# Optimization experiments

Measured on AMD Instinct MI355X. Metric: run time of the kernel, lower is better.

## Reference

```python
import jax, jax.numpy as jnp
import numpy as np

INPUT_DIM = 1024
HIDDEN = 64
NUM_MEM = 8   # +1 shared slot -> 9 total
K = 2
SEQ = 256
BATCH = 32


def setup_inputs() -> dict:
    key = jax.random.key(0)
    ks = jax.random.split(key, 10)
    s = 1.0 / np.sqrt(INPUT_DIM)
    nm1 = NUM_MEM + 1
    return {
        "X": jax.random.normal(ks[0], (SEQ, BATCH, INPUT_DIM), jnp.float32),
        "M_0": jnp.zeros((BATCH, nm1, HIDDEN, HIDDEN), jnp.float32),
        "Wk_w": jax.random.uniform(ks[1], (HIDDEN * nm1, INPUT_DIM), jnp.float32, -s, s),
        "Wk_b": jax.random.uniform(ks[2], (HIDDEN * nm1,), jnp.float32, -s, s),
        "Wv_w": jax.random.uniform(ks[3], (HIDDEN * nm1, INPUT_DIM), jnp.float32, -s, s),
        "Wv_b": jax.random.uniform(ks[4], (HIDDEN * nm1,), jnp.float32, -s, s),
        "Wg_w": jax.random.uniform(ks[5], (NUM_MEM, INPUT_DIM), jnp.float32, -s, s),
        "Wg_b": jax.random.uniform(ks[6], (NUM_MEM,), jnp.float32, -s, s),
        "Wq_w": jax.random.uniform(ks[7], (HIDDEN, INPUT_DIM), jnp.float32, -s, s),
        "Wq_b": jax.random.uniform(ks[8], (HIDDEN,), jnp.float32, -s, s),
    }


def _mom_forward(X, M_0, Wk_w, Wk_b, Wv_w, Wv_b, Wg_w, Wg_b, Wq_w, Wq_b):
    B = X.shape[1]
    nm1 = NUM_MEM + 1
    b_idx = jnp.arange(B)[:, None]

    def step(M, x_t):
        # gating + top-k routing (sorted descending, like torch.topk)
        score = jax.nn.softmax(x_t @ Wg_w.T + Wg_b, axis=1)          # (B, NUM_MEM)
        m_scores, m_idx = jax.lax.top_k(score, K)                    # (B, K)
        idx_update = jnp.concatenate(
            [jnp.zeros((B, 1), jnp.int32), m_idx.astype(jnp.int32)], axis=1)  # (B, K+1)
        g = m_scores / jnp.sum(m_scores, axis=1, keepdims=True)     # (B, K)

        Mk = (x_t @ Wk_w.T + Wk_b).reshape(B, nm1, HIDDEN)          # (B, 9, H)
        Mv = (x_t @ Wv_w.T + Wv_b).reshape(B, nm1, HIDDEN)
        # only gather the K+1 routed outer products instead of all 9
        k_sel = jnp.take_along_axis(Mk, idx_update[:, :, None], axis=1)  # (B, K+1, H)
        v_sel = jnp.take_along_axis(Mv, idx_update[:, :, None], axis=1)
        src = k_sel[..., :, None] * v_sel[..., None, :]              # (B, K+1, H, H)
        M = M.at[b_idx, idx_update].add(src)                         # scatter-add (dupes accumulate)

        M_use = M[b_idx, m_idx]                                      # (B, K, H, H)
        M_out = jnp.einsum('bk,bkij->bij', g, M_use) + M[:, 0]       # add shared memory
        q = x_t @ Wq_w.T + Wq_b                                      # (B, H)
        o = jnp.einsum('bi,bij->bj', q, M_out)                       # (B, H)
        return M, o

    M_final, outputs = jax.lax.scan(step, M_0, X)
    return outputs, M_final


def reference(X, M_0, Wk_w, Wk_b, Wv_w, Wv_b, Wg_w, Wg_b, Wq_w, Wq_b):
    return _mom_forward(X, M_0, Wk_w, Wk_b, Wv_w, Wv_b, Wg_w, Wg_b, Wq_w, Wq_b)
```

## Files before the change

kernel.cpp:

```cpp
#include <hip/hip_runtime.h>
#include <stdint.h>

#define SEQ 256
#define BATCH 32
#define IN_DIM 1024
#define HID 64
#define NPAD 1280
#define ROWS (SEQ*BATCH)

#define XBF_OFF   0
#define DMH_OFF   0
#define WBF_OFF   16777216
#define BB_OFF    19398656
#define GATE_OFF  19403776
#define Y_OFF     19534848

#define NC 8
#define CHL 32

#define DM_CB_U32 18432

typedef __attribute__((ext_vector_type(8))) short short8;
typedef __attribute__((ext_vector_type(4))) float floatx4;

typedef const __attribute__((address_space(1))) unsigned int gas_u32;
typedef __attribute__((address_space(3))) unsigned int las_u32;
static __device__ __forceinline__ void gl_lds16(const void* g, void* l) {
  __builtin_amdgcn_global_load_lds((gas_u32*)g, (las_u32*)l, 16, 0, 0);
}

static __device__ __forceinline__ short f2bf(float f) {
  union { float f; uint32_t u; } a; a.f = f;
  uint32_t r = (a.u + 0x7FFFu + ((a.u >> 16) & 1u)) >> 16;
  return (short)r;
}
static __device__ __forceinline__ float bflo(uint32_t u){ return __uint_as_float(u << 16); }
static __device__ __forceinline__ float bfhi(uint32_t u){ return __uint_as_float(u & 0xffff0000u); }
static __device__ __forceinline__ float bfu(unsigned short us){ return __uint_as_float(((uint32_t)us) << 16); }

__global__ __launch_bounds__(256) void prep_gate_kernel(
    const float* __restrict__ X,
    const float* __restrict__ Wk, const float* __restrict__ bk,
    const float* __restrict__ Wv, const float* __restrict__ bv,
    const float* __restrict__ Wg, const float* __restrict__ bg,
    const float* __restrict__ Wq, const float* __restrict__ bq,
    short* __restrict__ Xbf, short* __restrict__ Wbf,
    float* __restrict__ bb, float4* __restrict__ gate)
{
  if (blockIdx.x < 2048) {
    const int lane = threadIdx.x & 63;
    const int row  = blockIdx.x * 4 + (threadIdx.x >> 6);
    const float* x = X + (int64_t)row * IN_DIM;
    short4* xb = (short4*)(Xbf + (int64_t)row * IN_DIM);

    float acc[8];
#pragma unroll
    for (int e = 0; e < 8; e++) acc[e] = 0.f;
#pragma unroll
    for (int i = 0; i < 4; i++) {
      const int off = i * 256 + lane * 4;
      float4 xv = *(const float4*)(x + off);
      short4 s4;
      s4.x = f2bf(xv.x); s4.y = f2bf(xv.y); s4.z = f2bf(xv.z); s4.w = f2bf(xv.w);
      xb[i * 64 + lane] = s4;
#pragma unroll
      for (int e = 0; e < 8; e++) {
        float4 wv = *(const float4*)(Wg + e * IN_DIM + off);
        acc[e] += xv.x * wv.x + xv.y * wv.y + xv.z * wv.z + xv.w * wv.w;
      }
    }
#pragma unroll
    for (int e = 0; e < 8; e++) {
#pragma unroll
      for (int m = 32; m >= 1; m >>= 1)
        acc[e] += __shfl_xor(acc[e], m);
      acc[e] += bg[e];
    }
    if (lane == 0) {
      int i0 = 0; float v0 = acc[0];
#pragma unroll
      for (int e = 1; e < 8; e++) if (acc[e] > v0) { v0 = acc[e]; i0 = e; }
      int i1 = -1; float v1 = -3.4e38f;
#pragma unroll
      for (int e = 0; e < 8; e++) if (e != i0 && acc[e] > v1) { v1 = acc[e]; i1 = e; }
      float e1 = __expf(v1 - v0);
      float inv = 1.f / (1.f + e1);
      gate[row] = make_float4(__int_as_float(i0), __int_as_float(i1), inv, e1 * inv);
    }
  } else {
    const int idx = (blockIdx.x - 2048) * 256 + threadIdx.x;
    const int NW4 = NPAD * IN_DIM / 4;
#pragma unroll
    for (int i = idx; i < NW4; i += 65536) {
      int e = i * 4;
      int r = e >> 10;
      int k = e & 1023;
      float4 x;
      if (r < 576)       x = *(const float4*)(Wk + (int64_t)r*1024 + k);
      else if (r < 1152) x = *(const float4*)(Wv + (int64_t)(r-576)*1024 + k);
      else if (r < 1216) x = *(const float4*)(Wq + (int64_t)(r-1152)*1024 + k);
      else               x = make_float4(0.f, 0.f, 0.f, 0.f);
      short4 s4;
      s4.x = f2bf(x.x); s4.y = f2bf(x.y); s4.z = f2bf(x.z); s4.w = f2bf(x.w);
      ((short4*)Wbf)[i] = s4;
    }
    if (idx < NPAD) {
      int r = idx; float v;
      if (r < 576)       v = bk[r];
      else if (r < 1152) v = bv[r - 576];
      else if (r < 1216) v = bq[r - 1152];
      else               v = 0.f;
      bb[r] = v;
    }
  }
}

__global__ __launch_bounds__(256) void gemm_kernel(
    const short* __restrict__ Xbf,
    const short* __restrict__ Wbf,
    const float* __restrict__ bb,
    unsigned short* __restrict__ Yb)
{
  __shared__ short As[128 * 32];
  __shared__ short Bs[128 * 32];

  const int tid  = threadIdx.x;
  const int lane = tid & 63;
  const int wv   = tid >> 6;
  const int quad = lane >> 4;
  const int cl   = lane & 15;
  const int wm   = wv & 1;
  const int wn   = wv >> 1;
  const int m0 = blockIdx.y * 128;
  const int n0 = blockIdx.x * 128;

  const int srow = wv * 32 + (lane >> 2);
  const int scol = (lane & 3) * 8;
  const short* gA = Xbf + (int64_t)(m0 + srow) * IN_DIM + scol;
  const short* gB = Wbf + (int64_t)(n0 + srow) * IN_DIM + scol;
  short* lA = As + (wv * 32) * 32;
  short* lB = Bs + (wv * 32) * 32;

  floatx4 acc[4][4];
#pragma unroll
  for (int i = 0; i < 4; i++)
#pragma unroll
    for (int k = 0; k < 4; k++) acc[i][k] = (floatx4){0.f, 0.f, 0.f, 0.f};

  for (int ks = 0; ks < IN_DIM; ks += 32) {
    gl_lds16(gA + ks,                lA);
    gl_lds16(gA + 16 * IN_DIM + ks,  lA + 16 * 32);
    gl_lds16(gB + ks,                lB);
    gl_lds16(gB + 16 * IN_DIM + ks,  lB + 16 * 32);
    __syncthreads();

    short8 bfrag[4], afrag[4];
#pragma unroll
    for (int nt = 0; nt < 4; nt++)
      bfrag[nt] = *(const short8*)(&Bs[(wn * 64 + nt * 16 + cl) * 32 + quad * 8]);
#pragma unroll
    for (int mt = 0; mt < 4; mt++)
      afrag[mt] = *(const short8*)(&As[(wm * 64 + mt * 16 + cl) * 32 + quad * 8]);
#pragma unroll
    for (int mt = 0; mt < 4; mt++)
#pragma unroll
      for (int nt = 0; nt < 4; nt++)
        acc[mt][nt] = __builtin_amdgcn_mfma_f32_16x16x32_bf16(afrag[mt], bfrag[nt], acc[mt][nt], 0, 0, 0);
    __syncthreads();
  }

#pragma unroll
  for (int nt = 0; nt < 4; nt++) {
    const int col = n0 + wn * 64 + nt * 16 + cl;
    const float bias = bb[col];
#pragma unroll
    for (int mt = 0; mt < 4; mt++) {
#pragma unroll
      for (int r = 0; r < 4; r++) {
        int row = m0 + wm * 64 + mt * 16 + quad * 4 + r;
        Yb[(int64_t)row * NPAD + col] = (unsigned short)f2bf(acc[mt][nt][r] + bias);
      }
    }
  }
}

__global__ __launch_bounds__(512) void mfma_chunk_kernel(
    const unsigned short* __restrict__ Yb, const float4* __restrict__ gate,
    unsigned short* __restrict__ DMu, float* __restrict__ out)
{
  __shared__ uint32_t Qs[32 * 32];
  __shared__ uint32_t Ks[96 * 32];
  __shared__ unsigned short Kts[64 * 104];
  __shared__ unsigned short Vts[64 * 104];
  __shared__ unsigned short Ps[32 * 104];
  __shared__ float4 gl[32];
  __shared__ uint32_t su[96];

  const int blk = blockIdx.x;
  const int c   = blk & 7;
  const int b   = blk >> 3;
  const int tid = threadIdx.x;
  const int lane = tid & 63;
  const int wv  = tid >> 6;
  const int quad = lane >> 4;
  const int cl  = lane & 15;
  const int t0  = c * CHL;

  if (tid < 32) {
    float4 g = gate[(t0 + tid) * BATCH + b];
    gl[tid] = g;
    su[3 * tid]     = 0u;
    su[3 * tid + 1] = (uint32_t)__float_as_int(g.x);
    su[3 * tid + 2] = (uint32_t)__float_as_int(g.y);
  }
  __syncthreads();

  for (int idx = tid; idx < 1536; idx += 512) {
    const int e = idx >> 4, d4 = idx & 15;
    const int s = (e * 171) >> 9;
    const int u = e - 3 * s;
    const int head = (u == 0) ? 0 : (int)su[3 * s + u];
    const unsigned short* Yr = Yb + ((int64_t)(t0 + s) * BATCH + b) * NPAD;
    uint2 kp = *(const uint2*)(Yr + head * 64 + 4 * d4);
    *(uint2*)&Ks[e * 32 + 2 * d4] = kp;
    Kts[(4 * d4)     * 104 + e] = (unsigned short)(kp.x & 0xffffu);
    Kts[(4 * d4 + 1) * 104 + e] = (unsigned short)(kp.x >> 16);
    Kts[(4 * d4 + 2) * 104 + e] = (unsigned short)(kp.y & 0xffffu);
    Kts[(4 * d4 + 3) * 104 + e] = (unsigned short)(kp.y >> 16);
    uint2 vp = *(const uint2*)(Yr + 576 + head * 64 + 4 * d4);
    Vts[(4 * d4)     * 104 + e] = (unsigned short)(vp.x & 0xffffu);
    Vts[(4 * d4 + 1) * 104 + e] = (unsigned short)(vp.x >> 16);
    Vts[(4 * d4 + 2) * 104 + e] = (unsigned short)(vp.y & 0xffffu);
    Vts[(4 * d4 + 3) * 104 + e] = (unsigned short)(vp.y >> 16);
  }
  {
    const int s = tid >> 4, d4 = tid & 15;
    const unsigned short* Yr = Yb + ((int64_t)(t0 + s) * BATCH + b) * NPAD;
    uint2 qp = *(const uint2*)(Yr + 1152 + 4 * d4);
    *(uint2*)&Qs[s * 32 + 2 * d4] = qp;
  }
  __syncthreads();

  const unsigned short* Qu = (const unsigned short*)Qs;
  const unsigned short* Ku = (const unsigned short*)Ks;

  for (int tileId = wv; tileId < 12; tileId += 8) {
    const int mt = tileId / 6, nt = tileId % 6;
    floatx4 acc = (floatx4){0.f, 0.f, 0.f, 0.f};
#pragma unroll
    for (int kc = 0; kc < 2; kc++) {
      short8 af = *(const short8*)(Qu + (mt * 16 + cl) * 64 + kc * 32 + quad * 8);
      short8 bf = *(const short8*)(Ku + (nt * 16 + cl) * 64 + kc * 32 + quad * 8);
      acc = __builtin_amdgcn_mfma_f32_16x16x32_bf16(af, bf, acc, 0, 0, 0);
    }
    const int e = nt * 16 + cl;
    const int s_e = (e * 171) >> 9;
    const int slot_e = (int)su[e];
#pragma unroll
    for (int r = 0; r < 4; r++) {
      const int t = mt * 16 + quad * 4 + r;
      float4 g = gl[t];
      const int i0t = __float_as_int(g.x), i1t = __float_as_int(g.y);
      float w = (slot_e == 0 ? 1.f : 0.f)
              + (slot_e == i0t ? g.z : 0.f)
              + (slot_e == i1t ? g.w : 0.f);
      w = (s_e <= t) ? w : 0.f;
      Ps[t * 104 + e] = (unsigned short)f2bf(w * acc[r]);
    }
  }
  __syncthreads();

  {
    const int tileId = wv;
    const int mt = tileId >> 2, nt = tileId & 3;
    floatx4 acc = (floatx4){0.f, 0.f, 0.f, 0.f};
#pragma unroll
    for (int kc = 0; kc < 3; kc++) {
      short8 af = *(const short8*)(Ps  + (mt * 16 + cl) * 104 + kc * 32 + quad * 8);
      short8 bf = *(const short8*)(Vts + (nt * 16 + cl) * 104 + kc * 32 + quad * 8);
      acc = __builtin_amdgcn_mfma_f32_16x16x32_bf16(af, bf, acc, 0, 0, 0);
    }
#pragma unroll
    for (int r = 0; r < 4; r++) {
      const int t = mt * 16 + quad * 4 + r, j = nt * 16 + cl;
      out[(int64_t)(t0 + t) * (BATCH * HID) + b * HID + j] = acc[r];
    }
  }

  uint32_t sreg[3][8];
#pragma unroll
  for (int kc = 0; kc < 3; kc++)
#pragma unroll
    for (int jj = 0; jj < 8; jj++)
      sreg[kc][jj] = su[kc * 32 + quad * 8 + jj];

  short8 afc[4][3];
#pragma unroll
  for (int mt = 0; mt < 4; mt++)
#pragma unroll
    for (int kc = 0; kc < 3; kc++)
      afc[mt][kc] = *(const short8*)(Kts + (mt * 16 + cl) * 104 + kc * 32 + quad * 8);

  unsigned short* dmb = DMu + ((int64_t)(c * 32 + b)) * 36864;
  union U8 { short8 s; uint32_t u[4]; };

  for (int uu = wv; uu < 36; uu += 8) {
    const int mi = uu >> 2, nt = uu & 3;
    uint32_t md[3][4];
#pragma unroll
    for (int kc = 0; kc < 3; kc++)
#pragma unroll
      for (int p = 0; p < 4; p++)
        md[kc][p] = ((sreg[kc][2 * p]     == (uint32_t)mi) ? 0x0000ffffu : 0u) |
                    ((sreg[kc][2 * p + 1] == (uint32_t)mi) ? 0xffff0000u : 0u);
    short8 bm[3];
#pragma unroll
    for (int kc = 0; kc < 3; kc++) {
      U8 vv; vv.s = *(const short8*)(Vts + (nt * 16 + cl) * 104 + kc * 32 + quad * 8);
      vv.u[0] &= md[kc][0]; vv.u[1] &= md[kc][1];
      vv.u[2] &= md[kc][2]; vv.u[3] &= md[kc][3];
      bm[kc] = vv.s;
    }
#pragma unroll
    for (int mt = 0; mt < 4; mt++) {
      floatx4 acc = (floatx4){0.f, 0.f, 0.f, 0.f};
#pragma unroll
      for (int kc = 0; kc < 3; kc++)
        acc = __builtin_amdgcn_mfma_f32_16x16x32_bf16(afc[mt][kc], bm[kc], acc, 0, 0, 0);
#pragma unroll
      for (int r = 0; r < 4; r++) {
        const int i = mt * 16 + quad * 4 + r, j = nt * 16 + cl;
        dmb[mi * 4096 + i * 64 + j] = (unsigned short)f2bf(acc[r]);
      }
    }
  }
}

__global__ void prefix_kernel(const float* __restrict__ M0, uint32_t* __restrict__ DMh,
                              float* __restrict__ out)
{
  int64_t e = (int64_t)blockIdx.x * blockDim.x + threadIdx.x;
  int b = (int)(e / DM_CB_U32);
  int r = (int)(e % DM_CB_U32);
  int m = r >> 11, rem = r & 2047, i = rem >> 5, jp = rem & 31;
  int64_t f32i = (int64_t)b * 36864 + m * 4096 + i * 64 + jp * 2;
  float run0 = M0[f32i], run1 = M0[f32i + 1];
  uint32_t u[NC];
#pragma unroll
  for (int cc = 0; cc < NC; cc++)
    u[cc] = DMh[((int64_t)(cc * 32 + b)) * DM_CB_U32 + r];
#pragma unroll
  for (int cc = 0; cc < NC; cc++) {
    int64_t idx = ((int64_t)(cc * 32 + b)) * DM_CB_U32 + r;
    DMh[idx] = ((uint32_t)(unsigned short)f2bf(run0)) |
               (((uint32_t)(unsigned short)f2bf(run1)) << 16);
    run0 += bflo(u[cc]); run1 += bfhi(u[cc]);
  }
  *(float2*)(out + (int64_t)SEQ * BATCH * HID + f32i) = make_float2(run0, run1);
}

__global__ __launch_bounds__(256) void corr_kernel(
    const unsigned short* __restrict__ Yb, const float4* __restrict__ gate,
    const uint32_t* __restrict__ DMh, float* __restrict__ out)
{
  __shared__ unsigned short MsbT[9 * 32 * 68];
  __shared__ float2 qb[32 * 32];
  __shared__ float4 gl[32];
  const int blk = blockIdx.x;
  const int c   = blk & 7;
  const int jh  = (blk >> 3) & 1;
  const int b   = blk >> 4;
  const int tid = threadIdx.x;
  const int t0  = c * CHL;

  if (tid < 32) gl[tid] = gate[(t0 + tid) * BATCH + b];
#pragma unroll
  for (int k = 0; k < 4; k++) {
    int f = tid + 256 * k;
    int t = f >> 5, p = f & 31;
    uint32_t u = *(const uint32_t*)(Yb + ((int64_t)(t0 + t) * BATCH + b) * NPAD + 1152 + 2 * p);
    qb[t * 32 + p] = make_float2(bflo(u), bfhi(u));
  }
  const uint32_t* dmb = DMh + ((int64_t)(c * 32 + b)) * DM_CB_U32;
#pragma unroll
  for (int k = 0; k < 36; k++) {
    int f = tid + 256 * k;
    int m = f >> 10, rem = f & 1023, i = rem >> 4, p = rem & 15;
    uint32_t u = dmb[m * 2048 + i * 32 + jh * 16 + p];
    MsbT[(m * 32 + 2 * p)     * 68 + i] = (unsigned short)(u & 0xffffu);
    MsbT[(m * 32 + 2 * p + 1) * 68 + i] = (unsigned short)(u >> 16);
  }
  __syncthreads();

  const int jj = tid & 31;
  const int tg = tid >> 5;
#pragma unroll
  for (int tt = 0; tt < 4; tt++) {
    const int t = tt * 8 + tg;
    float4 g = gl[t];
    const int i0 = __float_as_int(g.x), i1 = __float_as_int(g.y);
    const float g0 = g.z, g1 = g.w;
    const unsigned short* P0 = MsbT + (0  * 32 + jj) * 68;
    const unsigned short* Pa = MsbT + (i0 * 32 + jj) * 68;
    const unsigned short* Pb = MsbT + (i1 * 32 + jj) * 68;
    float acc = 0.f;
#pragma unroll 4
    for (int i4 = 0; i4 < 16; i4++) {
      float2 qq0 = qb[t * 32 + 2 * i4];
      float2 qq1 = qb[t * 32 + 2 * i4 + 1];
      uint2 a0 = *(const uint2*)(P0 + 4 * i4);
      uint2 aa = *(const uint2*)(Pa + 4 * i4);
      uint2 ab = *(const uint2*)(Pb + 4 * i4);
      acc += qq0.x * (bflo(a0.x) + g0 * bflo(aa.x) + g1 * bflo(ab.x));
      acc += qq0.y * (bfhi(a0.x) + g0 * bfhi(aa.x) + g1 * bfhi(ab.x));
      acc += qq1.x * (bflo(a0.y) + g0 * bflo(aa.y) + g1 * bflo(ab.y));
      acc += qq1.y * (bfhi(a0.y) + g0 * bfhi(aa.y) + g1 * bfhi(ab.y));
    }
    float* op = out + (int64_t)(t0 + t) * (BATCH * HID) + b * HID + jh * 32 + jj;
    *op += acc;
  }
}

extern "C" void kernel_launch(void* const* d_in, const int* in_sizes, int n_in,
                              void* d_out, int out_size, void* d_ws, size_t ws_size,
                              hipStream_t stream)
{
  const float* X  = (const float*)d_in[0];
  const float* M0 = (const float*)d_in[1];
  const float* Wk = (const float*)d_in[2];
  const float* bk = (const float*)d_in[3];
  const float* Wv = (const float*)d_in[4];
  const float* bv = (const float*)d_in[5];
  const float* Wg = (const float*)d_in[6];
  const float* bg = (const float*)d_in[7];
  const float* Wq = (const float*)d_in[8];
  const float* bq = (const float*)d_in[9];

  char* ws = (char*)d_ws;
  short*          Xbf  = (short*)(ws + XBF_OFF);
  short*          Wbf  = (short*)(ws + WBF_OFF);
  float*          bb   = (float*)(ws + BB_OFF);
  float4*         gate = (float4*)(ws + GATE_OFF);
  unsigned short* Yb   = (unsigned short*)(ws + Y_OFF);
  uint32_t*       DMh  = (uint32_t*)(ws + DMH_OFF);
  unsigned short* DMu  = (unsigned short*)(ws + DMH_OFF);
  float*          out  = (float*)d_out;

  prep_gate_kernel<<<2304, 256, 0, stream>>>(X, Wk, bk, Wv, bv, Wg, bg, Wq, bq,
                                             Xbf, Wbf, bb, gate);
  dim3 gg(NPAD / 128, ROWS / 128);
  gemm_kernel<<<gg, 256, 0, stream>>>(Xbf, Wbf, bb, Yb);
  mfma_chunk_kernel<<<32 * NC, 512, 0, stream>>>(Yb, gate, DMu, out);
  prefix_kernel<<<(32 * DM_CB_U32) / 256, 256, 0, stream>>>(M0, DMh, out);
  corr_kernel<<<32 * NC * 2, 256, 0, stream>>>(Yb, gate, DMh, out);
}
```

Measured before the change: 171.3 us.

## Compute only routed expert K/V projections via per-expert row lists

Replaces the dense GEMM over all 1280 output columns with a dense part covering only the shared slot and Q, plus a grouped GEMM per expert that gathers only the rows routed to that expert. A new list-building kernel uses atomics to bucket rows by their top-2 experts. The output is compacted to 448 columns per row, which shrinks downstream reads. This removes roughly two thirds of the projection FLOPs but adds an extra launch, atomic list construction, gathered row loads, and empty blocks that exit early.

```diff
diff --git a/kernel.cpp b/kernel.cpp
--- a/kernel.cpp
+++ b/kernel.cpp
@@ -5,8 +5,8 @@
 #define BATCH 32
 #define IN_DIM 1024
 #define HID 64
-#define NPAD 1280
 #define ROWS (SEQ*BATCH)
+#define YW 448
 
 #define XBF_OFF   0
 #define DMH_OFF   0
@@ -14,6 +14,8 @@
 #define BB_OFF    19398656
 #define GATE_OFF  19403776
 #define Y_OFF     19534848
+#define LIST_OFF  26874880
+#define CNT_OFF   27137024
 
 #define NC 8
 #define CHL 32
@@ -45,7 +47,8 @@
     const float* __restrict__ Wg, const float* __restrict__ bg,
     const float* __restrict__ Wq, const float* __restrict__ bq,
     short* __restrict__ Xbf, short* __restrict__ Wbf,
-    float* __restrict__ bb, float4* __restrict__ gate)
+    float* __restrict__ bb, float4* __restrict__ gate,
+    uint32_t* __restrict__ cnts)
 {
   if (blockIdx.x < 2048) {
     const int lane = threadIdx.x & 63;
@@ -89,7 +92,7 @@
     }
   } else {
     const int idx = (blockIdx.x - 2048) * 256 + threadIdx.x;
-    const int NW4 = NPAD * IN_DIM / 4;
+    const int NW4 = 1216 * IN_DIM / 4;
 #pragma unroll
     for (int i = idx; i < NW4; i += 65536) {
       int e = i * 4;
@@ -98,31 +101,42 @@
       float4 x;
       if (r < 576)       x = *(const float4*)(Wk + (int64_t)r*1024 + k);
       else if (r < 1152) x = *(const float4*)(Wv + (int64_t)(r-576)*1024 + k);
-      else if (r < 1216) x = *(const float4*)(Wq + (int64_t)(r-1152)*1024 + k);
-      else               x = make_float4(0.f, 0.f, 0.f, 0.f);
+      else               x = *(const float4*)(Wq + (int64_t)(r-1152)*1024 + k);
       short4 s4;
       s4.x = f2bf(x.x); s4.y = f2bf(x.y); s4.z = f2bf(x.z); s4.w = f2bf(x.w);
       ((short4*)Wbf)[i] = s4;
     }
-    if (idx < NPAD) {
+    if (idx < 1216) {
       int r = idx; float v;
       if (r < 576)       v = bk[r];
       else if (r < 1152) v = bv[r - 576];
-      else if (r < 1216) v = bq[r - 1152];
-      else               v = 0.f;
+      else               v = bq[r - 1152];
       bb[r] = v;
     }
-  }
-}
-
-__global__ __launch_bounds__(256) void gemm_kernel(
-    const short* __restrict__ Xbf,
-    const short* __restrict__ Wbf,
-    const float* __restrict__ bb,
-    unsigned short* __restrict__ Yb)
+    if (idx < 8) cnts[idx] = 0u;
+  }
+}
+
+__global__ __launch_bounds__(256) void listbuild_kernel(
+    const float4* __restrict__ gate, uint32_t* __restrict__ lists, uint32_t* __restrict__ cnts)
+{
+  const int row = blockIdx.x * 256 + threadIdx.x;
+  float4 g = gate[row];
+  const int i0 = __float_as_int(g.x), i1 = __float_as_int(g.y);
+  uint32_t p0 = atomicAdd(&cnts[i0], 1u);
+  lists[i0 * 8192 + p0] = (uint32_t)row;
+  uint32_t p1 = atomicAdd(&cnts[i1], 1u);
+  lists[i1 * 8192 + p1] = (uint32_t)row | (1u << 13);
+}
+
+__global__ __launch_bounds__(256) void gemm2_kernel(
+    const short* __restrict__ Xbf, const short* __restrict__ Wbf,
+    const float* __restrict__ bb, const uint32_t* __restrict__ lists,
+    const uint32_t* __restrict__ cnts, unsigned short* __restrict__ Yc)
 {
   __shared__ short As[128 * 32];
-  __shared__ short Bs[128 * 32];
+  __shared__ short Bs[192 * 32];
+  __shared__ uint32_t rl[128];
 
   const int tid  = threadIdx.x;
   const int lane = tid & 63;
@@ -131,54 +145,124 @@
   const int cl   = lane & 15;
   const int wm   = wv & 1;
   const int wn   = wv >> 1;
-  const int m0 = blockIdx.y * 128;
-  const int n0 = blockIdx.x * 128;
-
-  const int srow = wv * 32 + (lane >> 2);
-  const int scol = (lane & 3) * 8;
-  const short* gA = Xbf + (int64_t)(m0 + srow) * IN_DIM + scol;
-  const short* gB = Wbf + (int64_t)(n0 + srow) * IN_DIM + scol;
-  short* lA = As + (wv * 32) * 32;
-  short* lB = Bs + (wv * 32) * 32;
-
-  floatx4 acc[4][4];
-#pragma unroll
-  for (int i = 0; i < 4; i++)
-#pragma unroll
-    for (int k = 0; k < 4; k++) acc[i][k] = (floatx4){0.f, 0.f, 0.f, 0.f};
-
-  for (int ks = 0; ks < IN_DIM; ks += 32) {
-    gl_lds16(gA + ks,                lA);
-    gl_lds16(gA + 16 * IN_DIM + ks,  lA + 16 * 32);
-    gl_lds16(gB + ks,                lB);
-    gl_lds16(gB + 16 * IN_DIM + ks,  lB + 16 * 32);
+  const int srow16 = lane >> 2;
+  const int scol   = (lane & 3) * 8;
+
+  if (blockIdx.x < 128) {
+    const int m0 = blockIdx.x * 64;
+    const short* gA = Xbf + (int64_t)(m0 + wv * 16 + srow16) * IN_DIM + scol;
+    const short* gB[3];
+#pragma unroll
+    for (int i = 0; i < 3; i++) {
+      const int b16 = (wv * 3 + i) * 16;
+      const int sb = b16 < 64 ? b16 : (b16 < 128 ? 512 + b16 : 1024 + b16);
+      gB[i] = Wbf + (int64_t)(sb + srow16) * IN_DIM + scol;
+    }
+    floatx4 acc[2][6];
+#pragma unroll
+    for (int i = 0; i < 2; i++)
+#pragma unroll
+      for (int k = 0; k < 6; k++) acc[i][k] = (floatx4){0.f, 0.f, 0.f, 0.f};
+
+    for (int ks = 0; ks < IN_DIM; ks += 32) {
+      gl_lds16(gA + ks, As + (wv * 16) * 32);
+#pragma unroll
+      for (int i = 0; i < 3; i++)
+        gl_lds16(gB[i] + ks, Bs + ((wv * 3 + i) * 16) * 32);
+      __syncthreads();
+      short8 af[2], bf[6];
+#pragma unroll
+      for (int mt = 0; mt < 2; mt++)
+        af[mt] = *(const short8*)(&As[(wm * 32 + mt * 16 + cl) * 32 + quad * 8]);
+#pragma unroll
+      for (int nt = 0; nt < 6; nt++)
+        bf[nt] = *(const short8*)(&Bs[(wn * 96 + nt * 16 + cl) * 32 + quad * 8]);
+#pragma unroll
+      for (int mt = 0; mt < 2; mt++)
+#pragma unroll
+        for (int nt = 0; nt < 6; nt++)
+          acc[mt][nt] = __builtin_amdgcn_mfma_f32_16x16x32_bf16(af[mt], bf[nt], acc[mt][nt], 0, 0, 0);
+      __syncthreads();
+    }
+#pragma unroll
+    for (int nt = 0; nt < 6; nt++) {
+      const int bcol = wn * 96 + nt * 16 + cl;
+      const float bias = bb[bcol < 64 ? bcol : (bcol < 128 ? 512 + bcol : 1024 + bcol)];
+      const int dest = (bcol & 63) + 192 * (bcol >> 6);
+#pragma unroll
+      for (int mt = 0; mt < 2; mt++) {
+#pragma unroll
+        for (int r = 0; r < 4; r++) {
+          const int row = m0 + wm * 32 + mt * 16 + quad * 4 + r;
+          Yc[(int64_t)row * YW + dest] = (unsigned short)f2bf(acc[mt][nt][r] + bias);
+        }
+      }
+    }
+  } else {
+    const int hb = blockIdx.x - 128;
+    const int h  = hb >> 6;
+    const int bo = (hb & 63) * 128;
+    const uint32_t cnt = cnts[h];
+    if ((uint32_t)bo >= cnt) return;
+
+    if (tid < 128) {
+      uint32_t e = ((uint32_t)(bo + tid) < cnt) ? lists[h * 8192 + bo + tid] : 0xFFFFFFFFu;
+      rl[tid] = e;
+    }
     __syncthreads();
 
-    short8 bfrag[4], afrag[4];
-#pragma unroll
-    for (int nt = 0; nt < 4; nt++)
-      bfrag[nt] = *(const short8*)(&Bs[(wn * 64 + nt * 16 + cl) * 32 + quad * 8]);
-#pragma unroll
-    for (int mt = 0; mt < 4; mt++)
-      afrag[mt] = *(const short8*)(&As[(wm * 64 + mt * 16 + cl) * 32 + quad * 8]);
-#pragma unroll
-    for (int mt = 0; mt < 4; mt++)
+    uint32_t eA0 = rl[wv * 32 + srow16];
+    uint32_t eA1 = rl[wv * 32 + 16 + srow16];
+    const short* gA0 = Xbf + (int64_t)(eA0 == 0xFFFFFFFFu ? 0 : (eA0 & 8191)) * IN_DIM + scol;
+    const short* gA1 = Xbf + (int64_t)(eA1 == 0xFFFFFFFFu ? 0 : (eA1 & 8191)) * IN_DIM + scol;
+    const int b16a = wv * 32, b16b = wv * 32 + 16;
+    const short* gB0 = Wbf + (int64_t)((b16a < 64 ? 64 * h + b16a : 512 + 64 * h + b16a) + srow16) * IN_DIM + scol;
+    const short* gB1 = Wbf + (int64_t)((b16b < 64 ? 64 * h + b16b : 512 + 64 * h + b16b) + srow16) * IN_DIM + scol;
+
+    floatx4 acc[4][4];
+#pragma unroll
+    for (int i = 0; i < 4; i++)
+#pragma unroll
+      for (int k = 0; k < 4; k++) acc[i][k] = (floatx4){0.f, 0.f, 0.f, 0.f};
+
+    for (int ks = 0; ks < IN_DIM; ks += 32) {
+      gl_lds16(gA0 + ks, As + (wv * 32) * 32);
+      gl_lds16(gA1 + ks, As + (wv * 32 + 16) * 32);
+      gl_lds16(gB0 + ks, Bs + (wv * 32) * 32);
+      gl_lds16(gB1 + ks, Bs + (wv * 32 + 16) * 32);
+      __syncthreads();
+      short8 af[4], bf[4];
+#pragma unroll
+      for (int mt = 0; mt < 4; mt++)
+        af[mt] = *(const short8*)(&As[(wm * 64 + mt * 16 + cl) * 32 + quad * 8]);
 #pragma unroll
       for (int nt = 0; nt < 4; nt++)
-        acc[mt][nt] = __builtin_amdgcn_mfma_f32_16x16x32_bf16(afrag[mt], bfrag[nt], acc[mt][nt], 0, 0, 0);
-    __syncthreads();
-  }
-
-#pragma unroll
-  for (int nt = 0; nt < 4; nt++) {
-    const int col = n0 + wn * 64 + nt * 16 + cl;
-    const float bias = bb[col];
-#pragma unroll
-    for (int mt = 0; mt < 4; mt++) {
-#pragma unroll
-      for (int r = 0; r < 4; r++) {
-        int row = m0 + wm * 64 + mt * 16 + quad * 4 + r;
-        Yb[(int64_t)row * NPAD + col] = (unsigned short)f2bf(acc[mt][nt][r] + bias);
+        bf[nt] = *(const short8*)(&Bs[(wn * 64 + nt * 16 + cl) * 32 + quad * 8]);
+#pragma unroll
+      for (int mt = 0; mt < 4; mt++)
+#pragma unroll
+        for (int nt = 0; nt < 4; nt++)
+          acc[mt][nt] = __builtin_amdgcn_mfma_f32_16x16x32_bf16(af[mt], bf[nt], acc[mt][nt], 0, 0, 0);
+      __syncthreads();
+    }
+#pragma unroll
+    for (int nt = 0; nt < 4; nt++) {
+      const int bcol = wn * 64 + nt * 16 + cl;
+      const float bias = bb[bcol < 64 ? 64 * h + bcol : 512 + 64 * h + bcol];
+#pragma unroll
+      for (int mt = 0; mt < 4; mt++) {
+#pragma unroll
+        for (int r = 0; r < 4; r++) {
+          const int rr = wm * 64 + mt * 16 + quad * 4 + r;
+          const uint32_t e = rl[rr];
+          if (e != 0xFFFFFFFFu) {
+            const int row = e & 8191;
+            const int j = (e >> 13) & 1;
+            const int dest = (bcol < 64) ? (64 + 64 * j + bcol)
+                                         : (256 + 64 * j + (bcol - 64));
+            Yc[(int64_t)row * YW + dest] = (unsigned short)f2bf(acc[mt][nt][r] + bias);
+          }
+        }
       }
     }
   }
@@ -213,21 +297,19 @@
     su[3 * tid + 1] = (uint32_t)__float_as_int(g.x);
     su[3 * tid + 2] = (uint32_t)__float_as_int(g.y);
   }
-  __syncthreads();
 
   for (int idx = tid; idx < 1536; idx += 512) {
     const int e = idx >> 4, d4 = idx & 15;
     const int s = (e * 171) >> 9;
     const int u = e - 3 * s;
-    const int head = (u == 0) ? 0 : (int)su[3 * s + u];
-    const unsigned short* Yr = Yb + ((int64_t)(t0 + s) * BATCH + b) * NPAD;
-    uint2 kp = *(const uint2*)(Yr + head * 64 + 4 * d4);
+    const unsigned short* Yr = Yb + ((int64_t)(t0 + s) * BATCH + b) * YW;
+    uint2 kp = *(const uint2*)(Yr + 64 * u + 4 * d4);
     *(uint2*)&Ks[e * 32 + 2 * d4] = kp;
     Kts[(4 * d4)     * 104 + e] = (unsigned short)(kp.x & 0xffffu);
     Kts[(4 * d4 + 1) * 104 + e] = (unsigned short)(kp.x >> 16);
     Kts[(4 * d4 + 2) * 104 + e] = (unsigned short)(kp.y & 0xffffu);
     Kts[(4 * d4 + 3) * 104 + e] = (unsigned short)(kp.y >> 16);
-    uint2 vp = *(const uint2*)(Yr + 576 + head * 64 + 4 * d4);
+    uint2 vp = *(const uint2*)(Yr + 192 + 64 * u + 4 * d4);
     Vts[(4 * d4)     * 104 + e] = (unsigned short)(vp.x & 0xffffu);
     Vts[(4 * d4 + 1) * 104 + e] = (unsigned short)(vp.x >> 16);
     Vts[(4 * d4 + 2) * 104 + e] = (unsigned short)(vp.y & 0xffffu);
@@ -235,8 +317,8 @@
   }
   {
     const int s = tid >> 4, d4 = tid & 15;
-    const unsigned short* Yr = Yb + ((int64_t)(t0 + s) * BATCH + b) * NPAD;
-    uint2 qp = *(const uint2*)(Yr + 1152 + 4 * d4);
+    const unsigned short* Yr = Yb + ((int64_t)(t0 + s) * BATCH + b) * YW;
+    uint2 qp = *(const uint2*)(Yr + 384 + 4 * d4);
     *(uint2*)&Qs[s * 32 + 2 * d4] = qp;
   }
   __syncthreads();
@@ -378,7 +460,7 @@
   for (int k = 0; k < 4; k++) {
     int f = tid + 256 * k;
     int t = f >> 5, p = f & 31;
-    uint32_t u = *(const uint32_t*)(Yb + ((int64_t)(t0 + t) * BATCH + b) * NPAD + 1152 + 2 * p);
+    uint32_t u = *(const uint32_t*)(Yb + ((int64_t)(t0 + t) * BATCH + b) * YW + 384 + 2 * p);
     qb[t * 32 + p] = make_float2(bflo(u), bfhi(u));
   }
   const uint32_t* dmb = DMh + ((int64_t)(c * 32 + b)) * DM_CB_U32;
@@ -437,20 +519,22 @@
   const float* bq = (const float*)d_in[9];
 
   char* ws = (char*)d_ws;
-  short*          Xbf  = (short*)(ws + XBF_OFF);
-  short*          Wbf  = (short*)(ws + WBF_OFF);
-  float*          bb   = (float*)(ws + BB_OFF);
-  float4*         gate = (float4*)(ws + GATE_OFF);
-  unsigned short* Yb   = (unsigned short*)(ws + Y_OFF);
-  uint32_t*       DMh  = (uint32_t*)(ws + DMH_OFF);
-  unsigned short* DMu  = (unsigned short*)(ws + DMH_OFF);
-  float*          out  = (float*)d_out;
+  short*          Xbf   = (short*)(ws + XBF_OFF);
+  short*          Wbf   = (short*)(ws + WBF_OFF);
+  float*          bb    = (float*)(ws + BB_OFF);
+  float4*         gate  = (float4*)(ws + GATE_OFF);
+  unsigned short* Yc    = (unsigned short*)(ws + Y_OFF);
+  uint32_t*       lists = (uint32_t*)(ws + LIST_OFF);
+  uint32_t*       cnts  = (uint32_t*)(ws + CNT_OFF);
+  uint32_t*       DMh   = (uint32_t*)(ws + DMH_OFF);
+  unsigned short* DMu   = (unsigned short*)(ws + DMH_OFF);
+  float*          out   = (float*)d_out;
 
   prep_gate_kernel<<<2304, 256, 0, stream>>>(X, Wk, bk, Wv, bv, Wg, bg, Wq, bq,
-                                             Xbf, Wbf, bb, gate);
-  dim3 gg(NPAD / 128, ROWS / 128);
-  gemm_kernel<<<gg, 256, 0, stream>>>(Xbf, Wbf, bb, Yb);
-  mfma_chunk_kernel<<<32 * NC, 512, 0, stream>>>(Yb, gate, DMu, out);
+                                             Xbf, Wbf, bb, gate, cnts);
+  listbuild_kernel<<<32, 256, 0, stream>>>(gate, lists, cnts);
+  gemm2_kernel<<<640, 256, 0, stream>>>(Xbf, Wbf, bb, lists, cnts, Yc);
+  mfma_chunk_kernel<<<32 * NC, 512, 0, stream>>>(Yc, gate, DMu, out);
   prefix_kernel<<<(32 * DM_CB_U32) / 256, 256, 0, stream>>>(M0, DMh, out);
-  corr_kernel<<<32 * NC * 2, 256, 0, stream>>>(Yb, gate, DMh, out);
-}
+  corr_kernel<<<32 * NC * 2, 256, 0, stream>>>(Yc, gate, DMh, out);
+}
```

Result: slower. 238.9 us (+39.4%).
